# Kernel optimization log

Measured on AMD Instinct MI355X. Metric: run time of the kernel, lower is better.

The kernel has to match this reference:

```python
import jax, jax.numpy as jnp
import numpy as np


def setup_inputs() -> dict:
    key = jax.random.key(0)
    ks = jax.random.split(key, 8)
    B, C, H, W = 4, 256, 64, 64
    QP = 32  # query_planes = inplanes // 8
    x = jax.random.normal(ks[0], (B, C, H, W), dtype=jnp.float32)
    Wq = jax.random.normal(ks[1], (QP, C), dtype=jnp.float32) * (1.0 / np.sqrt(C))
    bq = jax.random.normal(ks[2], (QP,), dtype=jnp.float32) * 0.01
    Wk = jax.random.normal(ks[3], (QP, C), dtype=jnp.float32) * (1.0 / np.sqrt(C))
    bk = jax.random.normal(ks[4], (QP,), dtype=jnp.float32) * 0.01
    Wv = jax.random.normal(ks[5], (C, C), dtype=jnp.float32) * (1.0 / np.sqrt(C))
    bv = jax.random.normal(ks[6], (C,), dtype=jnp.float32) * 0.01
    gamma = jax.random.normal(ks[7], (), dtype=jnp.float32)
    return {"x": x, "Wq": Wq, "bq": bq, "Wk": Wk, "bk": bk,
            "Wv": Wv, "bv": bv, "gamma": gamma}


def reference(x, Wq, bq, Wk, bk, Wv, bv, gamma):
    B, C, H, W = x.shape
    N = H * W
    flat = x.reshape(B, C, N)                              # [B, C, N]
    # 1x1 Conv1d == pointwise linear over channel dim
    q = jnp.einsum('qc,bcn->bnq', Wq, flat) + bq[None, None, :]   # [B, N, QP] (already permuted)
    k = jnp.einsum('qc,bcn->bqn', Wk, flat) + bk[None, :, None]   # [B, QP, N]
    v = jnp.einsum('oc,bcn->bon', Wv, flat) + bv[None, :, None]   # [B, C, N]
    # scores[b, i, j] = <q_i, k_j>, NO 1/sqrt(d) scaling (as in source)
    scores = jnp.einsum('biq,bqj->bij', q, k)              # [B, N, N]
    # unusual softmax axis: dim=1 == over query positions i, per column j
    attn = jax.nn.softmax(scores, axis=1)                  # [B, N, N]
    out_attn = jnp.einsum('bcn,bnj->bcj', v, attn)         # [B, C, N]
    out_attn = out_attn.reshape(B, C, H, W)
    return gamma * out_attn + x
```

## Files before the change

### kernel.cpp

```cpp
#include <hip/hip_runtime.h>
#include <hip/hip_bf16.h>
#include <math.h>


#define NBATCH 4
#define CDIM   256
#define NSEQ   4096
#define QPDIM  32
#define LOG2E  1.44269504088896340736f

typedef _Float16 half8_t  __attribute__((ext_vector_type(8)));
typedef _Float16 half2_t  __attribute__((ext_vector_type(2)));
typedef float    floatx4  __attribute__((ext_vector_type(4)));
typedef float    floatx16 __attribute__((ext_vector_type(16)));

union H8 { half8_t h8; half2_t h2[4]; int i32[4]; };

__device__ inline half2_t pack_f16(float a, float b) {
    return __builtin_bit_cast(half2_t, __builtin_amdgcn_cvt_pkrtz(a, b));
}

__global__ __launch_bounds__(256) void wprep_kernel(
    const float* __restrict__ Wv, const float* __restrict__ Wq,
    const float* __restrict__ Wk, _Float16* __restrict__ wH)
{
    const int idx = blockIdx.x * 256 + threadIdx.x;
    const int e = idx * 8;
    const int r = e >> 8, c = e & 255;
    const float* src;
    float scale = 1.0f;
    if (r < 256)      src = Wv + (size_t)r * 256 + c;
    else if (r < 288) { src = Wq + (size_t)(r - 256) * 256 + c; scale = LOG2E; }
    else              src = Wk + (size_t)(r - 288) * 256 + c;
    float4 f0 = ((const float4*)src)[0];
    float4 f1 = ((const float4*)src)[1];
    half8_t h;
    h[0] = (_Float16)(f0.x * scale); h[1] = (_Float16)(f0.y * scale);
    h[2] = (_Float16)(f0.z * scale); h[3] = (_Float16)(f0.w * scale);
    h[4] = (_Float16)(f1.x * scale); h[5] = (_Float16)(f1.y * scale);
    h[6] = (_Float16)(f1.z * scale); h[7] = (_Float16)(f1.w * scale);
    *(half8_t*)(wH + (size_t)r * 256 + c) = h;
}

__global__ __launch_bounds__(256, 2) void qkv_kernel(
    const float* __restrict__ x, const _Float16* __restrict__ wH,
    const float* __restrict__ bq, const float* __restrict__ bk,
    const float* __restrict__ bv,
    _Float16* __restrict__ qH, _Float16* __restrict__ kH,
    _Float16* __restrict__ vHT)
{
    __shared__ _Float16 xT[32][264];

    const int blk  = blockIdx.x;
    const int slot = blk & 7;
    const int b    = slot >> 1;
    const int n0   = (((blk >> 3) << 1) | (slot & 1)) << 5;
    const int t    = threadIdx.x;
    const int w    = t >> 6;
    const int lane = t & 63;
    const int quad = lane >> 4;
    const int col  = lane & 15;

    {
        const int crow0 = t >> 3;
        const int npart = t & 7;
        #pragma unroll
        for (int pass = 0; pass < 8; ++pass) {
            const int c = pass * 32 + crow0;
            float4 f = *(const float4*)(
                x + ((size_t)(b * CDIM + c)) * NSEQ + n0 + npart * 4);
            xT[npart * 4 + 0][c] = (_Float16)f.x;
            xT[npart * 4 + 1][c] = (_Float16)f.y;
            xT[npart * 4 + 2][c] = (_Float16)f.z;
            xT[npart * 4 + 3][c] = (_Float16)f.w;
        }
    }
    __syncthreads();

    const int r0 = w * 80;
    floatx4 acc[5][2];
    #pragma unroll
    for (int mt = 0; mt < 5; ++mt)
        #pragma unroll
        for (int nt = 0; nt < 2; ++nt)
            acc[mt][nt] = (floatx4){0.f, 0.f, 0.f, 0.f};

    #pragma unroll
    for (int ks = 0; ks < 8; ++ks) {
        half8_t bf[2];
        #pragma unroll
        for (int nt = 0; nt < 2; ++nt)
            bf[nt] = *(const half8_t*)&xT[nt * 16 + col][ks * 32 + quad * 8];
        #pragma unroll
        for (int mt = 0; mt < 5; ++mt) {
            half8_t a = *(const half8_t*)(
                wH + (size_t)(r0 + mt * 16 + col) * 256 + ks * 32 + quad * 8);
            #pragma unroll
            for (int nt = 0; nt < 2; ++nt)
                acc[mt][nt] = __builtin_amdgcn_mfma_f32_16x16x32_f16(
                    a, bf[nt], acc[mt][nt], 0, 0, 0);
        }
    }

    #pragma unroll
    for (int mt = 0; mt < 5; ++mt) {
        const int gbase = r0 + mt * 16;
        const float* bp; int rl; float bscale = 1.0f;
        if (gbase < 256)      { bp = bv; rl = gbase; }
        else if (gbase < 288) { bp = bq; rl = gbase - 256; bscale = LOG2E; }
        else                  { bp = bk; rl = gbase - 288; }
        #pragma unroll
        for (int reg = 0; reg < 4; ++reg) {
            const int rr = rl + quad * 4 + reg;
            const float bias = bp[rr] * bscale;
            #pragma unroll
            for (int nt = 0; nt < 2; ++nt) {
                const int n = n0 + nt * 16 + col;
                const float val = acc[mt][nt][reg] + bias;
                if (gbase < 256)
                    vHT[((size_t)(b * CDIM + rr)) * NSEQ + n] = (_Float16)val;
                else if (gbase < 288)
                    qH[((size_t)(b * NSEQ + n)) * QPDIM + rr] = (_Float16)val;
                else
                    kH[((size_t)(b * NSEQ + n)) * QPDIM + rr] = (_Float16)val;
            }
        }
    }
}

__global__ __launch_bounds__(256, 4) void mpass_kernel(
    const _Float16* __restrict__ qH, const _Float16* __restrict__ kH,
    float* __restrict__ ms4)
{
    __shared__ float wmax[4][32];

    const int blk  = blockIdx.x;
    const int slot = blk & 7;
    const int b    = slot >> 1;
    const int idx  = ((blk >> 3) << 1) | (slot & 1);
    const int jblk = idx & 63;
    const int iq   = idx >> 6;
    const int t    = threadIdx.x;
    const int w    = t >> 6;
    const int lane = t & 63;
    const int l5   = lane >> 5;
    const int lj   = lane & 31;
    const int jt   = w & 1, ih = w >> 1;

    const _Float16* qg = qH + (size_t)b * NSEQ * QPDIM;
    const int j = jblk * 64 + jt * 32 + lj;
    const half8_t kb0 = *(const half8_t*)(
        kH + ((size_t)(b * NSEQ + j)) * QPDIM + l5 * 8);
    const half8_t kb1 = *(const half8_t*)(
        kH + ((size_t)(b * NSEQ + j)) * QPDIM + 16 + l5 * 8);

    float mx = -1e30f;
    const int ibase = iq * 1024 + ih * 512;
    for (int cc = 0; cc < 16; ++cc) {
        const _Float16* qp = qg + (size_t)(ibase + cc * 32 + lj) * QPDIM + l5 * 8;
        half8_t qa0 = *(const half8_t*)qp;
        half8_t qa1 = *(const half8_t*)(qp + 16);
        floatx16 S = __builtin_amdgcn_mfma_f32_32x32x16_f16(
            qa0, kb0, (floatx16){0.f}, 0, 0, 0);
        S = __builtin_amdgcn_mfma_f32_32x32x16_f16(qa1, kb1, S, 0, 0, 0);
        #pragma unroll
        for (int r = 0; r < 16; ++r) mx = fmaxf(mx, S[r]);
    }
    mx = fmaxf(mx, __shfl_xor(mx, 32));
    if (lane < 32) wmax[w][lane] = mx;
    __syncthreads();
    if (t < 64) {
        const int jt3 = t >> 5, c = t & 31;
        ms4[(size_t)iq * (NBATCH * NSEQ) + (size_t)b * NSEQ
            + jblk * 64 + jt3 * 32 + c] = fmaxf(wmax[jt3][c], wmax[jt3 + 2][c]);
    }
}

__global__ __launch_bounds__(256, 4) void attn_kernel(
    const _Float16* __restrict__ qH, const _Float16* __restrict__ kH,
    const _Float16* __restrict__ vHT, const float* __restrict__ ms4,
    const float* __restrict__ x, const float* __restrict__ gamma,
    float* __restrict__ out)
{
    __shared__ _Float16 vbuf[2][4096];
    __shared__ float lred2[2][2][32];

    const int blk  = blockIdx.x;
    const int slot = blk & 7;
    const int b    = slot >> 1;
    const int idx  = ((blk >> 3) << 1) | (slot & 1);
    const int cb   = idx >> 6;
    const int jblk = idx & 63;
    const int j0   = jblk << 6;
    const int c0   = cb << 6;
    const int t    = threadIdx.x;
    const int w    = t >> 6;
    const int lane = t & 63;
    const int l5   = lane >> 5;
    const int lj   = lane & 31;
    const int jh   = w & 1;
    const int ih   = w >> 1;

    const _Float16* qg = qH + (size_t)b * NSEQ * QPDIM;
    const _Float16* vg = vHT + (size_t)b * CDIM * NSEQ;

    const int jme = j0 + jh * 32 + lj;
    const half8_t kb0 = *(const half8_t*)(
        kH + ((size_t)(b * NSEQ + jme)) * QPDIM + l5 * 8);
    const half8_t kb1 = *(const half8_t*)(
        kH + ((size_t)(b * NSEQ + jme)) * QPDIM + 16 + l5 * 8);
    const float* msb = ms4 + (size_t)b * NSEQ + jme;
    const float mfix = fmaxf(
        fmaxf(msb[0], msb[NBATCH * NSEQ]),
        fmaxf(msb[2 * NBATCH * NSEQ], msb[3 * NBATCH * NSEQ]));

    floatx16 acc[2];
    #pragma unroll
    for (int ct = 0; ct < 2; ++ct) acc[ct] = (floatx16){0.f};
    float lp = 0.0f;

    #define DMA_V(i0_, buf_)                                                   \
        {                                                                      \
            _Pragma("unroll")                                                  \
            for (int g = 0; g < 2; ++g) {                                      \
                const int uu = w * 128 + g * 64 + lane;                        \
                const int cl = uu >> 3;                                        \
                const int ck = (uu & 7) ^ (cl & 7);                            \
                const _Float16* src =                                          \
                    vg + (size_t)(c0 + cl) * NSEQ + (i0_) + ck * 8;            \
                __builtin_amdgcn_global_load_lds(                              \
                    (const __attribute__((address_space(1))) void*)src,        \
                    (__attribute__((address_space(3))) void*)                  \
                        (&vbuf[buf_][(w * 128 + g * 64) * 8]),                 \
                    16, 0, 0);                                                 \
            }                                                                  \
        }

    DMA_V(0, 0);
    const _Float16* qb = qg + (size_t)(ih * 32 + lj) * QPDIM + l5 * 8;
    half8_t qa0 = *(const half8_t*)(qb);
    half8_t qa1 = *(const half8_t*)(qb + 16);

    int cur = 0;
    for (int i0 = 0; i0 < NSEQ; i0 += 64) {
        __syncthreads();
        if (i0 + 64 < NSEQ) DMA_V(i0 + 64, cur ^ 1);

        floatx16 S = __builtin_amdgcn_mfma_f32_32x32x16_f16(
            qa0, kb0, (floatx16){0.f}, 0, 0, 0);
        S = __builtin_amdgcn_mfma_f32_32x32x16_f16(qa1, kb1, S, 0, 0, 0);

        H8 lo, hi;
        float ls = 0.0f;
        #pragma unroll
        for (int p = 0; p < 4; ++p) {
            float pa = __builtin_amdgcn_exp2f(S[2 * p]     - mfix);
            float pb = __builtin_amdgcn_exp2f(S[2 * p + 1] - mfix);
            ls += pa + pb;
            lo.h2[p] = pack_f16(pa, pb);
        }
        #pragma unroll
        for (int p = 0; p < 4; ++p) {
            float pa = __builtin_amdgcn_exp2f(S[8 + 2 * p]     - mfix);
            float pb = __builtin_amdgcn_exp2f(S[8 + 2 * p + 1] - mfix);
            ls += pa + pb;
            hi.h2[p] = pack_f16(pa, pb);
        }
        lp += ls;

        H8 P0, P1;
#if __has_builtin(__builtin_amdgcn_permlane32_swap)
        {
            auto r0p = __builtin_amdgcn_permlane32_swap(
                (unsigned)lo.i32[0], (unsigned)lo.i32[2], false, false);
            P0.i32[0] = (int)r0p[0]; P0.i32[2] = (int)r0p[1];
            auto r1p = __builtin_amdgcn_permlane32_swap(
                (unsigned)lo.i32[1], (unsigned)lo.i32[3], false, false);
            P0.i32[1] = (int)r1p[0]; P0.i32[3] = (int)r1p[1];
            auto r2p = __builtin_amdgcn_permlane32_swap(
                (unsigned)hi.i32[0], (unsigned)hi.i32[2], false, false);
            P1.i32[0] = (int)r2p[0]; P1.i32[2] = (int)r2p[1];
            auto r3p = __builtin_amdgcn_permlane32_swap(
                (unsigned)hi.i32[1], (unsigned)hi.i32[3], false, false);
            P1.i32[1] = (int)r3p[0]; P1.i32[3] = (int)r3p[1];
        }
#else
        {
            H8 shl, shh;
            #pragma unroll
            for (int r = 0; r < 4; ++r) {
                shl.i32[r] = __shfl_xor(lo.i32[r], 32);
                shh.i32[r] = __shfl_xor(hi.i32[r], 32);
            }
            const bool high = (l5 != 0);
            P0.i32[0] = high ? shl.i32[2] : lo.i32[0];
            P0.i32[1] = high ? shl.i32[3] : lo.i32[1];
            P0.i32[2] = high ? lo.i32[2]  : shl.i32[0];
            P0.i32[3] = high ? lo.i32[3]  : shl.i32[1];
            P1.i32[0] = high ? shh.i32[2] : hi.i32[0];
            P1.i32[1] = high ? shh.i32[3] : hi.i32[1];
            P1.i32[2] = high ? hi.i32[2]  : shh.i32[0];
            P1.i32[3] = high ? hi.i32[3]  : shh.i32[1];
        }
#endif

        #pragma unroll
        for (int ct = 0; ct < 2; ++ct) {
            const int cl = ct * 32 + lj;
            const int ic0 = (ih * 4 + 0 + l5) ^ (cl & 7);
            const int ic1 = (ih * 4 + 2 + l5) ^ (cl & 7);
            half8_t va0 = *(const half8_t*)&vbuf[cur][(cl * 8 + ic0) * 8];
            half8_t va1 = *(const half8_t*)&vbuf[cur][(cl * 8 + ic1) * 8];
            acc[ct] = __builtin_amdgcn_mfma_f32_32x32x16_f16(
                va0, P0.h8, acc[ct], 0, 0, 0);
            acc[ct] = __builtin_amdgcn_mfma_f32_32x32x16_f16(
                va1, P1.h8, acc[ct], 0, 0, 0);
        }

        if (i0 + 64 < NSEQ) {
            qa0 = *(const half8_t*)(qb + (size_t)(i0 + 64) * QPDIM);
            qa1 = *(const half8_t*)(qb + (size_t)(i0 + 64) * QPDIM + 16);
        }
        cur ^= 1;
    }

    lp += __shfl_xor(lp, 32);
    if (lane < 32) lred2[jh][ih][lane] = lp;
    __syncthreads();

    float* fred = (float*)vbuf;
    if (ih == 1) {
        #pragma unroll
        for (int ct = 0; ct < 2; ++ct)
            #pragma unroll
            for (int reg = 0; reg < 16; ++reg) {
                const int crow = (reg & 3) + 8 * (reg >> 2) + 4 * l5;
                fred[(ct * 32 + crow) * 64 + jh * 32 + lj] = acc[ct][reg];
            }
    }
    __syncthreads();

    if (ih == 0) {
        const float rv = gamma[0] / (lred2[jh][0][lj] + lred2[jh][1][lj]);
        #pragma unroll
        for (int ct = 0; ct < 2; ++ct) {
            #pragma unroll
            for (int reg = 0; reg < 16; ++reg) {
                const int crow = (reg & 3) + 8 * (reg >> 2) + 4 * l5;
                const int c_ = c0 + ct * 32 + crow;
                const size_t off = ((size_t)(b * CDIM + c_)) * NSEQ + jme;
                const float sum =
                    acc[ct][reg] + fred[(ct * 32 + crow) * 64 + jh * 32 + lj];
                out[off] = sum * rv + x[off];
            }
        }
    }
}

extern "C" void kernel_launch(void* const* d_in, const int* in_sizes, int n_in,
                              void* d_out, int out_size, void* d_ws, size_t ws_size,
                              hipStream_t stream) {
    const float* x     = (const float*)d_in[0];
    const float* Wq    = (const float*)d_in[1];
    const float* bq    = (const float*)d_in[2];
    const float* Wk    = (const float*)d_in[3];
    const float* bk    = (const float*)d_in[4];
    const float* Wv    = (const float*)d_in[5];
    const float* bv    = (const float*)d_in[6];
    const float* gamma = (const float*)d_in[7];
    float* out = (float*)d_out;

    _Float16* w16 = (_Float16*)d_ws;
    _Float16* qH  = w16;
    _Float16* kH  = qH + (size_t)NBATCH * NSEQ * QPDIM;
    _Float16* vHT = kH + (size_t)NBATCH * NSEQ * QPDIM;
    _Float16* wH  = vHT + (size_t)NBATCH * CDIM * NSEQ;
    float*    ms4 = (float*)(wH + (size_t)320 * 256);

    wprep_kernel<<<40, 256, 0, stream>>>(Wv, Wq, Wk, wH);
    qkv_kernel<<<512, 256, 0, stream>>>(x, wH, bq, bk, bv, qH, kH, vHT);
    mpass_kernel<<<1024, 256, 0, stream>>>(qH, kH, ms4);
    attn_kernel<<<1024, 256, 0, stream>>>(qH, kH, vHT, ms4, x, gamma, out);
}
```

Baseline: 178.7 us.

## Replace separate max pass with online softmax using lazy rescaling threshold

Removes the mpass kernel that precomputed the per-column maximum score and computes a running max inside the attention loop instead. Rescaling of the accumulators is done only when the tile max exceeds the running max by a threshold, which avoids frequent rescales. The row sums are accumulated with an extra MFMA against a ones vector rather than with scalar adds, and s_setprio is raised around the MFMA block. This trades a full recompute of QK^T for a per-iteration max reduction, a cross-lane shuffle, a wave-wide branch, extra MFMAs and a final merge of the two half-maxes.

```diff
diff --git a/kernel.cpp b/kernel.cpp
--- a/kernel.cpp
+++ b/kernel.cpp
@@ -8,6 +8,7 @@
 #define NSEQ   4096
 #define QPDIM  32
 #define LOG2E  1.44269504088896340736f
+#define RTHR   6.0f
 
 typedef _Float16 half8_t  __attribute__((ext_vector_type(8)));
 typedef _Float16 half2_t  __attribute__((ext_vector_type(2)));
@@ -128,62 +129,15 @@
     }
 }
 
-__global__ __launch_bounds__(256, 4) void mpass_kernel(
-    const _Float16* __restrict__ qH, const _Float16* __restrict__ kH,
-    float* __restrict__ ms4)
-{
-    __shared__ float wmax[4][32];
-
-    const int blk  = blockIdx.x;
-    const int slot = blk & 7;
-    const int b    = slot >> 1;
-    const int idx  = ((blk >> 3) << 1) | (slot & 1);
-    const int jblk = idx & 63;
-    const int iq   = idx >> 6;
-    const int t    = threadIdx.x;
-    const int w    = t >> 6;
-    const int lane = t & 63;
-    const int l5   = lane >> 5;
-    const int lj   = lane & 31;
-    const int jt   = w & 1, ih = w >> 1;
-
-    const _Float16* qg = qH + (size_t)b * NSEQ * QPDIM;
-    const int j = jblk * 64 + jt * 32 + lj;
-    const half8_t kb0 = *(const half8_t*)(
-        kH + ((size_t)(b * NSEQ + j)) * QPDIM + l5 * 8);
-    const half8_t kb1 = *(const half8_t*)(
-        kH + ((size_t)(b * NSEQ + j)) * QPDIM + 16 + l5 * 8);
-
-    float mx = -1e30f;
-    const int ibase = iq * 1024 + ih * 512;
-    for (int cc = 0; cc < 16; ++cc) {
-        const _Float16* qp = qg + (size_t)(ibase + cc * 32 + lj) * QPDIM + l5 * 8;
-        half8_t qa0 = *(const half8_t*)qp;
-        half8_t qa1 = *(const half8_t*)(qp + 16);
-        floatx16 S = __builtin_amdgcn_mfma_f32_32x32x16_f16(
-            qa0, kb0, (floatx16){0.f}, 0, 0, 0);
-        S = __builtin_amdgcn_mfma_f32_32x32x16_f16(qa1, kb1, S, 0, 0, 0);
-        #pragma unroll
-        for (int r = 0; r < 16; ++r) mx = fmaxf(mx, S[r]);
-    }
-    mx = fmaxf(mx, __shfl_xor(mx, 32));
-    if (lane < 32) wmax[w][lane] = mx;
-    __syncthreads();
-    if (t < 64) {
-        const int jt3 = t >> 5, c = t & 31;
-        ms4[(size_t)iq * (NBATCH * NSEQ) + (size_t)b * NSEQ
-            + jblk * 64 + jt3 * 32 + c] = fmaxf(wmax[jt3][c], wmax[jt3 + 2][c]);
-    }
-}
-
 __global__ __launch_bounds__(256, 4) void attn_kernel(
     const _Float16* __restrict__ qH, const _Float16* __restrict__ kH,
-    const _Float16* __restrict__ vHT, const float* __restrict__ ms4,
+    const _Float16* __restrict__ vHT,
     const float* __restrict__ x, const float* __restrict__ gamma,
     float* __restrict__ out)
 {
     __shared__ _Float16 vbuf[2][4096];
     __shared__ float lred2[2][2][32];
+    __shared__ float mred2[2][2][32];
 
     const int blk  = blockIdx.x;
     const int slot = blk & 7;
@@ -209,15 +163,15 @@
         kH + ((size_t)(b * NSEQ + jme)) * QPDIM + l5 * 8);
     const half8_t kb1 = *(const half8_t*)(
         kH + ((size_t)(b * NSEQ + jme)) * QPDIM + 16 + l5 * 8);
-    const float* msb = ms4 + (size_t)b * NSEQ + jme;
-    const float mfix = fmaxf(
-        fmaxf(msb[0], msb[NBATCH * NSEQ]),
-        fmaxf(msb[2 * NBATCH * NSEQ], msb[3 * NBATCH * NSEQ]));
 
     floatx16 acc[2];
     #pragma unroll
     for (int ct = 0; ct < 2; ++ct) acc[ct] = (floatx16){0.f};
-    float lp = 0.0f;
+    floatx16 lacc = (floatx16){0.f};
+    float m = -1e30f;
+
+    const half8_t vones = {(_Float16)1, (_Float16)1, (_Float16)1, (_Float16)1,
+                           (_Float16)1, (_Float16)1, (_Float16)1, (_Float16)1};
 
     #define DMA_V(i0_, buf_)                                                   \
         {                                                                      \
@@ -250,23 +204,38 @@
             qa0, kb0, (floatx16){0.f}, 0, 0, 0);
         S = __builtin_amdgcn_mfma_f32_32x32x16_f16(qa1, kb1, S, 0, 0, 0);
 
+        float t0 = fmaxf(fmaxf(S[0],  S[1]),  S[2]);
+        float t1 = fmaxf(fmaxf(S[3],  S[4]),  S[5]);
+        float t2 = fmaxf(fmaxf(S[6],  S[7]),  S[8]);
+        float t3 = fmaxf(fmaxf(S[9],  S[10]), S[11]);
+        float t4 = fmaxf(fmaxf(S[12], S[13]), S[14]);
+        float tm = fmaxf(fmaxf(fmaxf(t0, t1), fmaxf(t2, t3)),
+                         fmaxf(t4, S[15]));
+        tm = fmaxf(tm, __shfl_xor(tm, 32));
+        if (__any(tm > m + RTHR)) {
+            const float mn = fmaxf(m, tm);
+            const float sc = __builtin_amdgcn_exp2f(m - mn);
+            #pragma unroll
+            for (int ct = 0; ct < 2; ++ct)
+                #pragma unroll
+                for (int r = 0; r < 16; ++r) acc[ct][r] *= sc;
+            lacc[0] *= sc;
+            m = mn;
+        }
+
         H8 lo, hi;
-        float ls = 0.0f;
         #pragma unroll
         for (int p = 0; p < 4; ++p) {
-            float pa = __builtin_amdgcn_exp2f(S[2 * p]     - mfix);
-            float pb = __builtin_amdgcn_exp2f(S[2 * p + 1] - mfix);
-            ls += pa + pb;
+            float pa = __builtin_amdgcn_exp2f(S[2 * p]     - m);
+            float pb = __builtin_amdgcn_exp2f(S[2 * p + 1] - m);
             lo.h2[p] = pack_f16(pa, pb);
         }
         #pragma unroll
         for (int p = 0; p < 4; ++p) {
-            float pa = __builtin_amdgcn_exp2f(S[8 + 2 * p]     - mfix);
-            float pb = __builtin_amdgcn_exp2f(S[8 + 2 * p + 1] - mfix);
-            ls += pa + pb;
+            float pa = __builtin_amdgcn_exp2f(S[8 + 2 * p]     - m);
+            float pb = __builtin_amdgcn_exp2f(S[8 + 2 * p + 1] - m);
             hi.h2[p] = pack_f16(pa, pb);
         }
-        lp += ls;
 
         H8 P0, P1;
 #if __has_builtin(__builtin_amdgcn_permlane32_swap)
@@ -304,6 +273,11 @@
         }
 #endif
 
+        __builtin_amdgcn_s_setprio(1);
+        lacc = __builtin_amdgcn_mfma_f32_32x32x16_f16(
+            vones, P0.h8, lacc, 0, 0, 0);
+        lacc = __builtin_amdgcn_mfma_f32_32x32x16_f16(
+            vones, P1.h8, lacc, 0, 0, 0);
         #pragma unroll
         for (int ct = 0; ct < 2; ++ct) {
             const int cl = ct * 32 + lj;
@@ -316,6 +290,7 @@
             acc[ct] = __builtin_amdgcn_mfma_f32_32x32x16_f16(
                 va1, P1.h8, acc[ct], 0, 0, 0);
         }
+        __builtin_amdgcn_s_setprio(0);
 
         if (i0 + 64 < NSEQ) {
             qa0 = *(const half8_t*)(qb + (size_t)(i0 + 64) * QPDIM);
@@ -324,9 +299,17 @@
         cur ^= 1;
     }
 
-    lp += __shfl_xor(lp, 32);
-    if (lane < 32) lred2[jh][ih][lane] = lp;
+    if (lane < 32) mred2[jh][ih][lane] = m;
     __syncthreads();
+
+    const float mo = mred2[jh][ih ^ 1][lj];
+    const float M  = fmaxf(m, mo);
+    const float sc = __builtin_amdgcn_exp2f(m - M);
+    if (lane < 32) lred2[jh][ih][lane] = lacc[0] * sc;
+    #pragma unroll
+    for (int ct = 0; ct < 2; ++ct)
+        #pragma unroll
+        for (int r = 0; r < 16; ++r) acc[ct][r] *= sc;
 
     float* fred = (float*)vbuf;
     if (ih == 1) {
@@ -375,10 +358,8 @@
     _Float16* kH  = qH + (size_t)NBATCH * NSEQ * QPDIM;
     _Float16* vHT = kH + (size_t)NBATCH * NSEQ * QPDIM;
     _Float16* wH  = vHT + (size_t)NBATCH * CDIM * NSEQ;
-    float*    ms4 = (float*)(wH + (size_t)320 * 256);
 
     wprep_kernel<<<40, 256, 0, stream>>>(Wv, Wq, Wk, wH);
     qkv_kernel<<<512, 256, 0, stream>>>(x, wH, bq, bk, bv, qH, kH, vHT);
-    mpass_kernel<<<1024, 256, 0, stream>>>(qH, kH, ms4);
-    attn_kernel<<<1024, 256, 0, stream>>>(qH, kH, vHT, ms4, x, gamma, out);
-}
+    attn_kernel<<<1024, 256, 0, stream>>>(qH, kH, vHT, x, gamma, out);
+}
```

Measured after the change: 188.1 us. 5.3% more time.

## Share score tiles across 128 channels per block and sum rows with MFMA

Applied to the files above, without the earlier changes.

The attention block grows to 512 threads covering 128 output channels instead of 64, so each QK score tile and its exponentials are computed once for twice as many channels. The max subtraction moves into the MFMA accumulator initial value. The per-column softmax denominator is now accumulated by an MFMA against a ones vector instead of scalar adds and shuffles. The PV MFMA section is wrapped in s_setprio. Shared memory doubles and the launch bound of 512 threads with 4 blocks per CU may squeeze registers or reduce occupancy.

```diff
diff --git a/kernel.cpp b/kernel.cpp
--- a/kernel.cpp
+++ b/kernel.cpp
@@ -176,13 +176,13 @@
     }
 }
 
-__global__ __launch_bounds__(256, 4) void attn_kernel(
+__global__ __launch_bounds__(512, 4) void attn_kernel(
     const _Float16* __restrict__ qH, const _Float16* __restrict__ kH,
     const _Float16* __restrict__ vHT, const float* __restrict__ ms4,
     const float* __restrict__ x, const float* __restrict__ gamma,
     float* __restrict__ out)
 {
-    __shared__ _Float16 vbuf[2][4096];
+    __shared__ _Float16 vbuf[2][8192];
     __shared__ float lred2[2][2][32];
 
     const int blk  = blockIdx.x;
@@ -192,14 +192,15 @@
     const int cb   = idx >> 6;
     const int jblk = idx & 63;
     const int j0   = jblk << 6;
-    const int c0   = cb << 6;
+    const int c0   = cb << 7;
     const int t    = threadIdx.x;
     const int w    = t >> 6;
     const int lane = t & 63;
     const int l5   = lane >> 5;
     const int lj   = lane & 31;
     const int jh   = w & 1;
-    const int ih   = w >> 1;
+    const int ih   = (w >> 1) & 1;
+    const int ch   = w >> 2;
 
     const _Float16* qg = qH + (size_t)b * NSEQ * QPDIM;
     const _Float16* vg = vHT + (size_t)b * CDIM * NSEQ;
@@ -213,11 +214,17 @@
     const float mfix = fmaxf(
         fmaxf(msb[0], msb[NBATCH * NSEQ]),
         fmaxf(msb[2 * NBATCH * NSEQ], msb[3 * NBATCH * NSEQ]));
+    floatx16 Sinit;
+    #pragma unroll
+    for (int r = 0; r < 16; ++r) Sinit[r] = -mfix;
 
     floatx16 acc[2];
     #pragma unroll
     for (int ct = 0; ct < 2; ++ct) acc[ct] = (floatx16){0.f};
-    float lp = 0.0f;
+    floatx16 lacc = (floatx16){0.f};
+
+    const half8_t vones = {(_Float16)1, (_Float16)1, (_Float16)1, (_Float16)1,
+                           (_Float16)1, (_Float16)1, (_Float16)1, (_Float16)1};
 
     #define DMA_V(i0_, buf_)                                                   \
         {                                                                      \
@@ -247,26 +254,22 @@
         if (i0 + 64 < NSEQ) DMA_V(i0 + 64, cur ^ 1);
 
         floatx16 S = __builtin_amdgcn_mfma_f32_32x32x16_f16(
-            qa0, kb0, (floatx16){0.f}, 0, 0, 0);
+            qa0, kb0, Sinit, 0, 0, 0);
         S = __builtin_amdgcn_mfma_f32_32x32x16_f16(qa1, kb1, S, 0, 0, 0);
 
         H8 lo, hi;
-        float ls = 0.0f;
         #pragma unroll
         for (int p = 0; p < 4; ++p) {
-            float pa = __builtin_amdgcn_exp2f(S[2 * p]     - mfix);
-            float pb = __builtin_amdgcn_exp2f(S[2 * p + 1] - mfix);
-            ls += pa + pb;
+            float pa = __builtin_amdgcn_exp2f(S[2 * p]);
+            float pb = __builtin_amdgcn_exp2f(S[2 * p + 1]);
             lo.h2[p] = pack_f16(pa, pb);
         }
         #pragma unroll
         for (int p = 0; p < 4; ++p) {
-            float pa = __builtin_amdgcn_exp2f(S[8 + 2 * p]     - mfix);
-            float pb = __builtin_amdgcn_exp2f(S[8 + 2 * p + 1] - mfix);
-            ls += pa + pb;
+            float pa = __builtin_amdgcn_exp2f(S[8 + 2 * p]);
+            float pb = __builtin_amdgcn_exp2f(S[8 + 2 * p + 1]);
             hi.h2[p] = pack_f16(pa, pb);
         }
-        lp += ls;
 
         H8 P0, P1;
 #if __has_builtin(__builtin_amdgcn_permlane32_swap)
@@ -304,9 +307,14 @@
         }
 #endif
 
+        __builtin_amdgcn_s_setprio(1);
+        lacc = __builtin_amdgcn_mfma_f32_32x32x16_f16(
+            vones, P0.h8, lacc, 0, 0, 0);
+        lacc = __builtin_amdgcn_mfma_f32_32x32x16_f16(
+            vones, P1.h8, lacc, 0, 0, 0);
         #pragma unroll
         for (int ct = 0; ct < 2; ++ct) {
-            const int cl = ct * 32 + lj;
+            const int cl = ch * 64 + ct * 32 + lj;
             const int ic0 = (ih * 4 + 0 + l5) ^ (cl & 7);
             const int ic1 = (ih * 4 + 2 + l5) ^ (cl & 7);
             half8_t va0 = *(const half8_t*)&vbuf[cur][(cl * 8 + ic0) * 8];
@@ -316,6 +324,7 @@
             acc[ct] = __builtin_amdgcn_mfma_f32_32x32x16_f16(
                 va1, P1.h8, acc[ct], 0, 0, 0);
         }
+        __builtin_amdgcn_s_setprio(0);
 
         if (i0 + 64 < NSEQ) {
             qa0 = *(const half8_t*)(qb + (size_t)(i0 + 64) * QPDIM);
@@ -324,8 +333,7 @@
         cur ^= 1;
     }
 
-    lp += __shfl_xor(lp, 32);
-    if (lane < 32) lred2[jh][ih][lane] = lp;
+    if (lane < 32) lred2[jh][ih][lane] = lacc[0];
     __syncthreads();
 
     float* fred = (float*)vbuf;
@@ -335,7 +343,8 @@
             #pragma unroll
             for (int reg = 0; reg < 16; ++reg) {
                 const int crow = (reg & 3) + 8 * (reg >> 2) + 4 * l5;
-                fred[(ct * 32 + crow) * 64 + jh * 32 + lj] = acc[ct][reg];
+                fred[(ch * 64 + ct * 32 + crow) * 64 + jh * 32 + lj] =
+                    acc[ct][reg];
             }
     }
     __syncthreads();
@@ -347,10 +356,10 @@
             #pragma unroll
             for (int reg = 0; reg < 16; ++reg) {
                 const int crow = (reg & 3) + 8 * (reg >> 2) + 4 * l5;
-                const int c_ = c0 + ct * 32 + crow;
+                const int c_ = c0 + ch * 64 + ct * 32 + crow;
                 const size_t off = ((size_t)(b * CDIM + c_)) * NSEQ + jme;
-                const float sum =
-                    acc[ct][reg] + fred[(ct * 32 + crow) * 64 + jh * 32 + lj];
+                const float sum = acc[ct][reg] +
+                    fred[(ch * 64 + ct * 32 + crow) * 64 + jh * 32 + lj];
                 out[off] = sum * rv + x[off];
             }
         }
@@ -380,5 +389,5 @@
     wprep_kernel<<<40, 256, 0, stream>>>(Wv, Wq, Wk, wH);
     qkv_kernel<<<512, 256, 0, stream>>>(x, wH, bq, bk, bv, qH, kH, vHT);
     mpass_kernel<<<1024, 256, 0, stream>>>(qH, kH, ms4);
-    attn_kernel<<<1024, 256, 0, stream>>>(qH, kH, vHT, ms4, x, gamma, out);
-}
+    attn_kernel<<<512, 512, 0, stream>>>(qH, kH, vHT, ms4, x, gamma, out);
+}
```

After: 178.5 us. No clear change (-0.1%).

## Compute all channels per block to share softmax weights across channel tiles

Applied to the files above, without the earlier changes.

Each attention block now covers all 256 output channels for a 64-column tile using 512 threads and a 128-row i step, instead of four separate channel-block launches. This removes the fourfold recomputation of QK scores and exponentials. The max subtraction is folded into the MFMA accumulator initial value, and MFMA issue gets raised wave priority. In exchange, the grid shrinks to 256 blocks, LDS use grows to 128KB and there are many more accumulator registers, which lowers occupancy. The cross-wave reduction also becomes a multi-stage LDS exchange.

```diff
diff --git a/kernel.cpp b/kernel.cpp
--- a/kernel.cpp
+++ b/kernel.cpp
@@ -176,23 +176,20 @@
     }
 }
 
-__global__ __launch_bounds__(256, 4) void attn_kernel(
+__global__ __launch_bounds__(512, 2) void attn_kernel(
     const _Float16* __restrict__ qH, const _Float16* __restrict__ kH,
     const _Float16* __restrict__ vHT, const float* __restrict__ ms4,
     const float* __restrict__ x, const float* __restrict__ gamma,
     float* __restrict__ out)
 {
-    __shared__ _Float16 vbuf[2][4096];
-    __shared__ float lred2[2][2][32];
+    __shared__ _Float16 vbuf[2][32768];
+    __shared__ float lred[2][4][32];
 
     const int blk  = blockIdx.x;
     const int slot = blk & 7;
     const int b    = slot >> 1;
-    const int idx  = ((blk >> 3) << 1) | (slot & 1);
-    const int cb   = idx >> 6;
-    const int jblk = idx & 63;
+    const int jblk = ((blk >> 3) << 1) | (slot & 1);
     const int j0   = jblk << 6;
-    const int c0   = cb << 6;
     const int t    = threadIdx.x;
     const int w    = t >> 6;
     const int lane = t & 63;
@@ -213,25 +210,28 @@
     const float mfix = fmaxf(
         fmaxf(msb[0], msb[NBATCH * NSEQ]),
         fmaxf(msb[2 * NBATCH * NSEQ], msb[3 * NBATCH * NSEQ]));
-
-    floatx16 acc[2];
+    floatx16 Sinit;
     #pragma unroll
-    for (int ct = 0; ct < 2; ++ct) acc[ct] = (floatx16){0.f};
+    for (int r = 0; r < 16; ++r) Sinit[r] = -mfix;
+
+    floatx16 acc[8];
+    #pragma unroll
+    for (int ct = 0; ct < 8; ++ct) acc[ct] = (floatx16){0.f};
     float lp = 0.0f;
 
     #define DMA_V(i0_, buf_)                                                   \
         {                                                                      \
             _Pragma("unroll")                                                  \
-            for (int g = 0; g < 2; ++g) {                                      \
-                const int uu = w * 128 + g * 64 + lane;                        \
-                const int cl = uu >> 3;                                        \
-                const int ck = (uu & 7) ^ (cl & 7);                            \
+            for (int g = 0; g < 8; ++g) {                                      \
+                const int uu = w * 512 + g * 64 + lane;                        \
+                const int cl = uu >> 4;                                        \
+                const int ck = (uu & 15) ^ (cl & 7);                           \
                 const _Float16* src =                                          \
-                    vg + (size_t)(c0 + cl) * NSEQ + (i0_) + ck * 8;            \
+                    vg + (size_t)cl * NSEQ + (i0_) + ck * 8;                   \
                 __builtin_amdgcn_global_load_lds(                              \
                     (const __attribute__((address_space(1))) void*)src,        \
                     (__attribute__((address_space(3))) void*)                  \
-                        (&vbuf[buf_][(w * 128 + g * 64) * 8]),                 \
+                        (&vbuf[buf_][(w * 512 + g * 64) * 8]),                 \
                     16, 0, 0);                                                 \
             }                                                                  \
         }
@@ -242,27 +242,27 @@
     half8_t qa1 = *(const half8_t*)(qb + 16);
 
     int cur = 0;
-    for (int i0 = 0; i0 < NSEQ; i0 += 64) {
+    for (int i0 = 0; i0 < NSEQ; i0 += 128) {
         __syncthreads();
-        if (i0 + 64 < NSEQ) DMA_V(i0 + 64, cur ^ 1);
+        if (i0 + 128 < NSEQ) DMA_V(i0 + 128, cur ^ 1);
 
         floatx16 S = __builtin_amdgcn_mfma_f32_32x32x16_f16(
-            qa0, kb0, (floatx16){0.f}, 0, 0, 0);
+            qa0, kb0, Sinit, 0, 0, 0);
         S = __builtin_amdgcn_mfma_f32_32x32x16_f16(qa1, kb1, S, 0, 0, 0);
 
         H8 lo, hi;
         float ls = 0.0f;
         #pragma unroll
         for (int p = 0; p < 4; ++p) {
-            float pa = __builtin_amdgcn_exp2f(S[2 * p]     - mfix);
-            float pb = __builtin_amdgcn_exp2f(S[2 * p + 1] - mfix);
+            float pa = __builtin_amdgcn_exp2f(S[2 * p]);
+            float pb = __builtin_amdgcn_exp2f(S[2 * p + 1]);
             ls += pa + pb;
             lo.h2[p] = pack_f16(pa, pb);
         }
         #pragma unroll
         for (int p = 0; p < 4; ++p) {
-            float pa = __builtin_amdgcn_exp2f(S[8 + 2 * p]     - mfix);
-            float pb = __builtin_amdgcn_exp2f(S[8 + 2 * p + 1] - mfix);
+            float pa = __builtin_amdgcn_exp2f(S[8 + 2 * p]);
+            float pb = __builtin_amdgcn_exp2f(S[8 + 2 * p + 1]);
             ls += pa + pb;
             hi.h2[p] = pack_f16(pa, pb);
         }
@@ -304,53 +304,92 @@
         }
 #endif
 
-        #pragma unroll
-        for (int ct = 0; ct < 2; ++ct) {
+        __builtin_amdgcn_s_setprio(1);
+        #pragma unroll
+        for (int ct = 0; ct < 8; ++ct) {
             const int cl = ct * 32 + lj;
             const int ic0 = (ih * 4 + 0 + l5) ^ (cl & 7);
             const int ic1 = (ih * 4 + 2 + l5) ^ (cl & 7);
-            half8_t va0 = *(const half8_t*)&vbuf[cur][(cl * 8 + ic0) * 8];
-            half8_t va1 = *(const half8_t*)&vbuf[cur][(cl * 8 + ic1) * 8];
+            half8_t va0 = *(const half8_t*)&vbuf[cur][(cl * 16 + ic0) * 8];
+            half8_t va1 = *(const half8_t*)&vbuf[cur][(cl * 16 + ic1) * 8];
             acc[ct] = __builtin_amdgcn_mfma_f32_32x32x16_f16(
                 va0, P0.h8, acc[ct], 0, 0, 0);
             acc[ct] = __builtin_amdgcn_mfma_f32_32x32x16_f16(
                 va1, P1.h8, acc[ct], 0, 0, 0);
         }
-
-        if (i0 + 64 < NSEQ) {
-            qa0 = *(const half8_t*)(qb + (size_t)(i0 + 64) * QPDIM);
-            qa1 = *(const half8_t*)(qb + (size_t)(i0 + 64) * QPDIM + 16);
+        __builtin_amdgcn_s_setprio(0);
+
+        if (i0 + 128 < NSEQ) {
+            qa0 = *(const half8_t*)(qb + (size_t)(i0 + 128) * QPDIM);
+            qa1 = *(const half8_t*)(qb + (size_t)(i0 + 128) * QPDIM + 16);
         }
         cur ^= 1;
     }
 
     lp += __shfl_xor(lp, 32);
-    if (lane < 32) lred2[jh][ih][lane] = lp;
+    if (lane < 32) lred[jh][ih][lane] = lp;
     __syncthreads();
 
     float* fred = (float*)vbuf;
-    if (ih == 1) {
-        #pragma unroll
-        for (int ct = 0; ct < 2; ++ct)
+    const int rA = jh * 2 + (ih >> 1);
+    if (ih & 1) {
+        float* rg = fred + rA * 8192;
+        #pragma unroll
+        for (int ct = 0; ct < 8; ++ct)
             #pragma unroll
             for (int reg = 0; reg < 16; ++reg) {
                 const int crow = (reg & 3) + 8 * (reg >> 2) + 4 * l5;
-                fred[(ct * 32 + crow) * 64 + jh * 32 + lj] = acc[ct][reg];
-            }
-    }
-    __syncthreads();
-
-    if (ih == 0) {
-        const float rv = gamma[0] / (lred2[jh][0][lj] + lred2[jh][1][lj]);
-        #pragma unroll
-        for (int ct = 0; ct < 2; ++ct) {
+                rg[(ct * 32 + crow) * 32 + lj] = acc[ct][reg];
+            }
+    }
+    __syncthreads();
+    if (!(ih & 1)) {
+        float* rg = fred + rA * 8192;
+        #pragma unroll
+        for (int ct = 0; ct < 8; ++ct)
             #pragma unroll
             for (int reg = 0; reg < 16; ++reg) {
                 const int crow = (reg & 3) + 8 * (reg >> 2) + 4 * l5;
-                const int c_ = c0 + ct * 32 + crow;
+                acc[ct][reg] += rg[(ct * 32 + crow) * 32 + lj];
+            }
+    }
+    __syncthreads();
+    if (ih == 0) {
+        float* rg = fred + (jh * 2 + 0) * 8192;
+        #pragma unroll
+        for (int ct = 4; ct < 8; ++ct)
+            #pragma unroll
+            for (int reg = 0; reg < 16; ++reg) {
+                const int crow = (reg & 3) + 8 * (reg >> 2) + 4 * l5;
+                rg[(ct * 32 + crow) * 32 + lj] = acc[ct][reg];
+            }
+    } else if (ih == 2) {
+        float* rg = fred + (jh * 2 + 1) * 8192;
+        #pragma unroll
+        for (int ct = 0; ct < 4; ++ct)
+            #pragma unroll
+            for (int reg = 0; reg < 16; ++reg) {
+                const int crow = (reg & 3) + 8 * (reg >> 2) + 4 * l5;
+                rg[(ct * 32 + crow) * 32 + lj] = acc[ct][reg];
+            }
+    }
+    __syncthreads();
+    if (ih == 0 || ih == 2) {
+        const float lsum = lred[jh][0][lj] + lred[jh][1][lj]
+                         + lred[jh][2][lj] + lred[jh][3][lj];
+        const float rv = gamma[0] / lsum;
+        const int ct0 = (ih == 0) ? 0 : 4;
+        float* rg = fred + (jh * 2 + ((ih == 0) ? 1 : 0)) * 8192;
+        #pragma unroll
+        for (int cc = 0; cc < 4; ++cc) {
+            const int ct = ct0 + cc;
+            #pragma unroll
+            for (int reg = 0; reg < 16; ++reg) {
+                const int crow = (reg & 3) + 8 * (reg >> 2) + 4 * l5;
+                const int c_ = ct * 32 + crow;
                 const size_t off = ((size_t)(b * CDIM + c_)) * NSEQ + jme;
                 const float sum =
-                    acc[ct][reg] + fred[(ct * 32 + crow) * 64 + jh * 32 + lj];
+                    acc[ct][reg] + rg[(ct * 32 + crow) * 32 + lj];
                 out[off] = sum * rv + x[off];
             }
         }
@@ -380,5 +419,5 @@
     wprep_kernel<<<40, 256, 0, stream>>>(Wv, Wq, Wk, wH);
     qkv_kernel<<<512, 256, 0, stream>>>(x, wH, bq, bk, bv, qH, kH, vHT);
     mpass_kernel<<<1024, 256, 0, stream>>>(qH, kH, ms4);
-    attn_kernel<<<1024, 256, 0, stream>>>(qH, kH, vHT, ms4, x, gamma, out);
-}
+    attn_kernel<<<256, 512, 0, stream>>>(qH, kH, vHT, ms4, x, gamma, out);
+}
```

New measurement: 430.8 us. 141% more time.
